# Kernel tuning notes

Measured on AMD Instinct MI355X. Metric: run time of the kernel, lower is better.

The kernel has to match this reference:

```python
import jax, jax.numpy as jnp
import numpy as np
import math

B, N, DIM = 4, 1024, 512
H, DH = 8, 64
INNER = H * DH
K_REG, TEMP = 0.3, 0.1
LARGE_NEG = -math.log(1e10)


def setup_inputs() -> dict:
    key = jax.random.key(0)
    ks = jax.random.split(key, 10)
    x = jax.random.normal(ks[0], (B, N, DIM), dtype=jnp.float32)
    # binary float mask [b, n, n]; keep diagonal on so every row has a positive pair
    mask = (jax.random.uniform(ks[1], (B, N, N)) < 0.5).astype(jnp.float32)
    mask = jnp.maximum(mask, jnp.eye(N, dtype=jnp.float32)[None])
    s_in = 1.0 / math.sqrt(DIM)
    s_out = 1.0 / math.sqrt(INNER)
    u = lambda k, shape, s: jax.random.uniform(k, shape, jnp.float32, -s, s)
    return {
        "x": x, "attn_mask": mask,
        "Wq": u(ks[2], (INNER, DIM), s_in), "bq": u(ks[3], (INNER,), s_in),
        "Wk": u(ks[4], (INNER, DIM), s_in), "bk": u(ks[5], (INNER,), s_in),
        "Wv": u(ks[6], (INNER, DIM), s_in), "bv": u(ks[7], (INNER,), s_in),
        "Wo": u(ks[8], (DIM, INNER), s_out), "bo": u(ks[9], (DIM,), s_out),
    }


def _dynamical_contrastive_loss(scores, attn_mask, norm_matrix):
    # reconstructed from CARD's DynamicalContrastiveLoss(k, temperature)
    n = scores.shape[-1]
    cos = scores / norm_matrix / TEMP                     # [b,h,n,n]
    m = jnp.max(cos, axis=-1, keepdims=True)              # stable exp; ratio unchanged
    e = jnp.exp(cos - m)
    amask = attn_mask[:, None]                            # [b,1,n,n]
    pos = jnp.sum(e * amask, axis=-1)                     # [b,h,n]
    allsum = jnp.sum(e, axis=-1)
    clustering = -jnp.log(pos / allsum)                   # [b,h,n]
    eye = jnp.eye(n, dtype=scores.dtype)
    regular = jnp.sum(jnp.abs(eye[None] - attn_mask), axis=(-2, -1)) / (n * (n - 1))  # [b]
    loss = jnp.mean(clustering, axis=(1, 2)) + K_REG * regular
    return jnp.mean(loss)


def reference(x, attn_mask, Wq, bq, Wk, bk, Wv, bv, Wo, bo):
    b, n, _ = x.shape
    split = lambda t: t.reshape(b, n, H, DH).transpose(0, 2, 1, 3)  # b h n d
    q = split(x @ Wq.T + bq)
    k = split(x @ Wk.T + bk)
    v = split(x @ Wv.T + bv)
    scores = jnp.einsum("bhid,bhjd->bhij", q, k)
    q_norm = jnp.linalg.norm(q, axis=-1, keepdims=True)   # [b,h,n,1]
    k_norm = jnp.linalg.norm(k, axis=-1, keepdims=True)
    norm_matrix = q_norm * jnp.swapaxes(k_norm, -1, -2)   # [b,h,n,n]
    amask = attn_mask[:, None]                            # [b,1,n,n]
    masked_scores = scores * amask + jnp.where(amask == 0, LARGE_NEG, 0.0)
    dcl = _dynamical_contrastive_loss(scores, attn_mask, norm_matrix)
    scale = 1.0 / math.sqrt(DH)
    attn = jax.nn.softmax(masked_scores * scale, axis=-1)
    out = jnp.einsum("bhij,bhjd->bhid", attn, v)
    out = out.transpose(0, 2, 1, 3).reshape(b, n, INNER)
    out = out @ Wo.T + bo                                 # dropout is identity at eval
    return out, attn, dcl
```

## Files before the change

### kernel.cpp

```cpp
#include <hip/hip_runtime.h>
#include <hip/hip_bf16.h>
#include <math.h>

#define NB 4
#define NN 1024
#define DIMD 512
#define NH 8
#define DHD 64
#define INNERD 512
#define SCALE 0.125f
#define TEMPP 0.1f
#define KREG 0.3f
#define LNEG -23.025850929940457f

typedef __attribute__((ext_vector_type(8))) short bf16x8;
typedef __attribute__((ext_vector_type(4))) short bf16x4;
typedef __attribute__((ext_vector_type(4))) float f32x4;

static __device__ __forceinline__ short f2bf(float f) {
  unsigned u = __float_as_uint(f);
  u += 0x7fffu + ((u >> 16) & 1u);
  return (short)(u >> 16);
}
static __device__ __forceinline__ float bf2f(short s) {
  unsigned u = ((unsigned)(unsigned short)s) << 16;
  return __uint_as_float(u);
}

static __device__ __forceinline__ float wave_sum(float v) {
#pragma unroll
  for (int o = 1; o < 64; o <<= 1) v += __shfl_xor(v, o, 64);
  return v;
}
static __device__ __forceinline__ float wave_min(float v) {
#pragma unroll
  for (int o = 1; o < 64; o <<= 1) v = fminf(v, __shfl_xor(v, o, 64));
  return v;
}

__global__ __launch_bounds__(256) void k_qkv(
    const float* __restrict__ x,
    const float* __restrict__ Wq, const float* __restrict__ bq,
    const float* __restrict__ Wk, const float* __restrict__ bk,
    const float* __restrict__ Wv, const float* __restrict__ bv,
    short* __restrict__ Qb, short* __restrict__ Kb, short* __restrict__ Vb,
    float* __restrict__ qn, float* __restrict__ kn) {
  __shared__ __align__(16) short As[64][40];
  __shared__ __align__(16) short Bs[64][40];
  const int tid = threadIdx.x;
  const int lane = tid & 63;
  const int wv = tid >> 6;
  const int m0 = blockIdx.x * 64;
  const int oc = blockIdx.y;
  const int which = oc >> 3;
  const int h = oc & 7;
  const float* W = (which == 0) ? Wq : (which == 1) ? Wk : Wv;
  const float* bias = (which == 0) ? bq : (which == 1) ? bk : bv;
  short* Out = (which == 0) ? Qb : (which == 1) ? Kb : Vb;
  const int o0 = h * 64;

  const f32x4 zero4 = {0.f, 0.f, 0.f, 0.f};
  f32x4 acc[4] = {zero4, zero4, zero4, zero4};

  const int sr = tid >> 3;
  const int sc = (tid & 7) * 4;

  for (int ks = 0; ks < 16; ++ks) {
    const int k0 = ks * 32;
    __syncthreads();
#pragma unroll
    for (int t = 0; t < 2; ++t) {
      const int r = sr + t * 32;
      const f32x4 va = *reinterpret_cast<const f32x4*>(&x[(m0 + r) * DIMD + k0 + sc]);
      const f32x4 vb = *reinterpret_cast<const f32x4*>(&W[(o0 + r) * DIMD + k0 + sc]);
      bf16x4 pa, pb;
#pragma unroll
      for (int i2 = 0; i2 < 4; ++i2) { pa[i2] = f2bf(va[i2]); pb[i2] = f2bf(vb[i2]); }
      *reinterpret_cast<bf16x4*>(&As[r][sc]) = pa;
      *reinterpret_cast<bf16x4*>(&Bs[r][sc]) = pb;
    }
    __syncthreads();
    const int kk = (lane >> 4) * 8;
    const bf16x8 a = *reinterpret_cast<const bf16x8*>(&As[wv * 16 + (lane & 15)][kk]);
#pragma unroll
    for (int n = 0; n < 4; ++n) {
      const bf16x8 b = *reinterpret_cast<const bf16x8*>(&Bs[n * 16 + (lane & 15)][kk]);
      acc[n] = __builtin_amdgcn_mfma_f32_16x16x32_bf16(a, b, acc[n], 0, 0, 0);
    }
  }

  const int colb = lane & 15;
  const int rbase = m0 + wv * 16 + ((lane >> 4) << 2);
  const int bidx = m0 >> 10;
  const int hb = (bidx * NH + h) << 10;
  float p2[4] = {0.f, 0.f, 0.f, 0.f};
#pragma unroll
  for (int n = 0; n < 4; ++n) {
    const float bval = bias[o0 + n * 16 + colb];
#pragma unroll
    for (int i = 0; i < 4; ++i) {
      const float val = acc[n][i] + bval;
      p2[i] += val * val;
      const int m = rbase + i;
      Out[(long)(hb + (m & (NN - 1))) * DHD + n * 16 + colb] = f2bf(val);
    }
  }
  if (which < 2) {
    float* norm = (which == 0) ? qn : kn;
#pragma unroll
    for (int off = 1; off < 16; off <<= 1) {
#pragma unroll
      for (int i = 0; i < 4; ++i) p2[i] += __shfl_xor(p2[i], off, 64);
    }
    if (colb == 0) {
#pragma unroll
      for (int i = 0; i < 4; ++i) {
        const int m = rbase + i;
        const float nv = sqrtf(p2[i]);
        norm[hb + (m & (NN - 1))] = (which == 0) ? (1.0f / (nv * TEMPP)) : (1.0f / nv);
      }
    }
  }
}

__global__ __launch_bounds__(256) void k_vtrans(const short* __restrict__ Vb,
                                                short* __restrict__ VbT) {
  __shared__ __align__(16) short T[64][72];
  const int tid = threadIdx.x;
  const int bh = blockIdx.y;
  const int j0 = blockIdx.x * 64;
#pragma unroll
  for (int t = 0; t < 2; ++t) {
    const int idx = tid + 256 * t;
    const int r = idx >> 3, c8 = (idx & 7) * 8;
    *reinterpret_cast<bf16x8*>(&T[r][c8]) =
        *reinterpret_cast<const bf16x8*>(&Vb[(long)((bh << 10) + j0 + r) * DHD + c8]);
  }
  __syncthreads();
  const int d = tid & 63;
  const int cg = tid >> 6;
#pragma unroll
  for (int t = 0; t < 2; ++t) {
    const int ch = cg * 2 + t;
    bf16x8 v;
#pragma unroll
    for (int jj = 0; jj < 8; ++jj) v[jj] = T[ch * 8 + jj][d];
    *reinterpret_cast<bf16x8*>(&VbT[((long)(bh * DHD + d) << 10) + j0 + ch * 8]) = v;
  }
}

__global__ __launch_bounds__(256) void k_kmax(const float* __restrict__ kn,
                                              float* __restrict__ kms) {
  const int tid = threadIdx.x;
  const int bh = blockIdx.x;
  const f32x4 v = *reinterpret_cast<const f32x4*>(&kn[(bh << 10) + tid * 4]);
  float m = fminf(fminf(v[0], v[1]), fminf(v[2], v[3]));
  m = wave_min(m);
  __shared__ float red[4];
  if ((tid & 63) == 0) red[tid >> 6] = m;
  __syncthreads();
  if (tid == 0) {
    const float mn = fminf(fminf(red[0], red[1]), fminf(red[2], red[3]));
    kms[bh] = (1.0f / mn) * SCALE / TEMPP;
  }
}

static __device__ __forceinline__ short* sp(short* S, int r, int c) {
  return (short*)((char*)S + (((r << 11) + (c << 1)) ^ ((r & 7) << 4)));
}

__global__ __launch_bounds__(256) void k_attn(
    const short* __restrict__ Qb, const short* __restrict__ Kb,
    const short* __restrict__ VbT,
    const float* __restrict__ mask,
    const float* __restrict__ qn, const float* __restrict__ kn,
    const float* __restrict__ kms,
    float* __restrict__ attn, short* __restrict__ AVb,
    float* __restrict__ partial, float* __restrict__ partial2) {
  __shared__ short S[16 * 1024];
  __shared__ float red[4][16][3];
  __shared__ float redc[4][16];
  __shared__ float rowv[16];
  __shared__ float rowscale[16];
  __shared__ float rowc[16];
  const int tid = threadIdx.x;
  const int lane = tid & 63;
  const int wv = tid >> 6;
  const int i0 = blockIdx.x * 16;
  const int bh = blockIdx.y;
  const int b = bh >> 3, h = bh & 7;

  const int lr = lane & 15;
  const int lk = lane >> 4;

  const long qoff = (long)((bh << 10) + i0 + lr) * DHD + lk * 8;
  const bf16x8 q0 = *reinterpret_cast<const bf16x8*>(&Qb[qoff]);
  const bf16x8 q1 = *reinterpret_cast<const bf16x8*>(&Qb[qoff + 32]);
  const short* Kbase = &Kb[(long)(bh << 10) * DHD];
  const float* mrow = mask + ((long)b << 20) + ((long)(i0 + lr) << 10);
  const float* knr = kn + (bh << 10);
  const float inv_qt = qn[(bh << 10) + i0 + lr];
  const float mlb = kms[bh] / inv_qt;
  const float argM = LNEG * SCALE - mlb;

  float Z = 0.f, alls = 0.f, pos = 0.f, cntf = 0.f;
#pragma unroll
  for (int jt = 0; jt < 16; ++jt) {
    const int j0 = wv * 256 + jt * 16;
    const long koff = (long)(j0 + lr) * DHD + lk * 8;
    const bf16x8 k0 = *reinterpret_cast<const bf16x8*>(&Kbase[koff]);
    const bf16x8 k1 = *reinterpret_cast<const bf16x8*>(&Kbase[koff + 32]);
    f32x4 acc = {0.f, 0.f, 0.f, 0.f};
    acc = __builtin_amdgcn_mfma_f32_16x16x32_bf16(k0, q0, acc, 0, 0, 0);
    acc = __builtin_amdgcn_mfma_f32_16x16x32_bf16(k1, q1, acc, 0, 0, 0);
    const int jl = j0 + lk * 4;
    const f32x4 mv = *reinterpret_cast<const f32x4*>(&mrow[jl]);
    const f32x4 kv = *reinterpret_cast<const f32x4*>(&knr[jl]);
    bf16x4 p;
#pragma unroll
    for (int e = 0; e < 4; ++e) {
      const float s = acc[e];
      const bool mset = (mv[e] != 0.0f);
      const float ev = __expf(mset ? (s * SCALE - mlb) : argM);
      const float ec = __expf(__builtin_fmaf(s * inv_qt, kv[e], -1.0f / TEMPP));
      Z += ev;
      alls += ec;
      pos += mset ? ec : 0.0f;
      cntf += mset ? 1.0f : 0.0f;
      p[e] = f2bf(ev);
    }
    *reinterpret_cast<bf16x4*>(sp(S, lr, jl)) = p;
  }
  Z += __shfl_xor(Z, 16, 64);    Z += __shfl_xor(Z, 32, 64);
  alls += __shfl_xor(alls, 16, 64); alls += __shfl_xor(alls, 32, 64);
  pos += __shfl_xor(pos, 16, 64);  pos += __shfl_xor(pos, 32, 64);
  if (lk == 0) { red[wv][lr][0] = Z; red[wv][lr][1] = alls; red[wv][lr][2] = pos; }
  if (h == 0) {
    cntf += __shfl_xor(cntf, 16, 64); cntf += __shfl_xor(cntf, 32, 64);
    if (lk == 0) redc[wv][lr] = cntf;
  }
  __syncthreads();

  const int r = tid >> 4, sub = tid & 15;
  if (sub == 0) {
    const float Zt = red[0][r][0] + red[1][r][0] + red[2][r][0] + red[3][r][0];
    const float at = red[0][r][1] + red[1][r][1] + red[2][r][1] + red[3][r][1];
    const float pt = red[0][r][2] + red[1][r][2] + red[2][r][2] + red[3][r][2];
    rowscale[r] = 1.0f / Zt;
    rowv[r] = __logf(at) - __logf(pt);
    if (h == 0) rowc[r] = redc[0][r] + redc[1][r] + redc[2][r] + redc[3][r];
  }
  __syncthreads();

  const float rZ = rowscale[r];
  float* arow = attn + ((long)bh << 20) + ((long)(i0 + r) << 10);
#pragma unroll
  for (int k = 0; k < 8; ++k) {
    const int c0 = sub * 8 + k * 128;
    const bf16x8 sv = *reinterpret_cast<const bf16x8*>(sp(S, r, c0));
    f32x4 o0, o1;
#pragma unroll
    for (int e = 0; e < 4; ++e) {
      o0[e] = bf2f(sv[e]) * rZ;
      o1[e] = bf2f(sv[4 + e]) * rZ;
    }
    *reinterpret_cast<f32x4*>(&arow[c0]) = o0;
    *reinterpret_cast<f32x4*>(&arow[c0 + 4]) = o1;
  }
  if (tid == 0) {
    float s = 0.f;
#pragma unroll
    for (int i = 0; i < 16; ++i) s += rowv[i];
    partial[bh * 64 + blockIdx.x] = s;
    if (h == 0) {
      float c = 0.f;
#pragma unroll
      for (int i = 0; i < 16; ++i) c += rowc[i];
      partial2[b * 64 + blockIdx.x] = c - 16.0f;
    }
  }

  f32x4 acc2 = {0.f, 0.f, 0.f, 0.f};
  const short* vrow = &VbT[(long)(bh * DHD + wv * 16 + lr) << 10];
#pragma unroll 8
  for (int k0 = 0; k0 < 32; ++k0) {
    const bf16x8 a = *reinterpret_cast<const bf16x8*>(sp(S, lr, k0 * 32 + lk * 8));
    const bf16x8 bb = *reinterpret_cast<const bf16x8*>(&vrow[k0 * 32 + lk * 8]);
    acc2 = __builtin_amdgcn_mfma_f32_16x16x32_bf16(a, bb, acc2, 0, 0, 0);
  }
#pragma unroll
  for (int i = 0; i < 4; ++i) {
    const int row = lk * 4 + i;
    const float o = acc2[i] * rowscale[row];
    AVb[((long)((b << 10) + i0 + row) << 9) + h * DHD + wv * 16 + lr] = f2bf(o);
  }
}

__global__ __launch_bounds__(256) void k_outproj(const short* __restrict__ AVb,
                                                 const float* __restrict__ Wo,
                                                 const float* __restrict__ bo,
                                                 float* __restrict__ out) {
  __shared__ __align__(16) short As[64][40];
  __shared__ __align__(16) short Bs[64][40];
  const int tid = threadIdx.x;
  const int lane = tid & 63, wv = tid >> 6;
  const int m0 = blockIdx.x * 64, o0 = blockIdx.y * 64;
  const f32x4 zero4 = {0.f, 0.f, 0.f, 0.f};
  f32x4 acc[4] = {zero4, zero4, zero4, zero4};
  const int ar = tid >> 2, ac = (tid & 3) * 8;
  const int br2 = tid >> 3, bc4 = (tid & 7) * 4;

  for (int ks = 0; ks < 16; ++ks) {
    const int k0 = ks * 32;
    __syncthreads();
    *reinterpret_cast<bf16x8*>(&As[ar][ac]) =
        *reinterpret_cast<const bf16x8*>(&AVb[((long)(m0 + ar) << 9) + k0 + ac]);
#pragma unroll
    for (int t = 0; t < 2; ++t) {
      const int rr = br2 + t * 32;
      const f32x4 vb = *reinterpret_cast<const f32x4*>(&Wo[(o0 + rr) * DIMD + k0 + bc4]);
      bf16x4 pbv;
#pragma unroll
      for (int i2 = 0; i2 < 4; ++i2) pbv[i2] = f2bf(vb[i2]);
      *reinterpret_cast<bf16x4*>(&Bs[rr][bc4]) = pbv;
    }
    __syncthreads();
    const int kk = (lane >> 4) * 8;
    const bf16x8 a = *reinterpret_cast<const bf16x8*>(&As[wv * 16 + (lane & 15)][kk]);
#pragma unroll
    for (int n = 0; n < 4; ++n) {
      const bf16x8 b = *reinterpret_cast<const bf16x8*>(&Bs[n * 16 + (lane & 15)][kk]);
      acc[n] = __builtin_amdgcn_mfma_f32_16x16x32_bf16(a, b, acc[n], 0, 0, 0);
    }
  }
  const int rbase = m0 + wv * 16 + ((lane >> 4) << 2);
#pragma unroll
  for (int i = 0; i < 4; ++i) {
#pragma unroll
    for (int n = 0; n < 4; ++n) {
      const int o = o0 + n * 16 + (lane & 15);
      out[((long)(rbase + i) << 9) + o] = acc[n][i] + bo[o];
    }
  }
}

__global__ __launch_bounds__(256) void k_finalize(const float* __restrict__ partial,
                                                  const float* __restrict__ partial2,
                                                  float* __restrict__ dcl) {
  const int tid = threadIdx.x;
  float s = 0.f;
#pragma unroll
  for (int t = 0; t < 8; ++t) s += partial[tid + t * 256];
  float s2 = partial2[tid];
  s = wave_sum(s);
  s2 = wave_sum(s2);
  __shared__ float red[4], red2[4];
  if ((tid & 63) == 0) { red[tid >> 6] = s; red2[tid >> 6] = s2; }
  __syncthreads();
  if (tid == 0) {
    const float cl = red[0] + red[1] + red[2] + red[3];
    const float rg = red2[0] + red2[1] + red2[2] + red2[3];
    *dcl = cl / (float)(NB * NH * NN) + KREG * rg / ((float)NN * (float)(NN - 1)) / (float)NB;
  }
}

extern "C" void kernel_launch(void* const* d_in, const int* in_sizes, int n_in,
                              void* d_out, int out_size, void* d_ws, size_t ws_size,
                              hipStream_t stream) {
  const float* x = (const float*)d_in[0];
  const float* mask = (const float*)d_in[1];
  const float* Wq = (const float*)d_in[2];
  const float* bq = (const float*)d_in[3];
  const float* Wk = (const float*)d_in[4];
  const float* bk = (const float*)d_in[5];
  const float* Wv = (const float*)d_in[6];
  const float* bv = (const float*)d_in[7];
  const float* Wo = (const float*)d_in[8];
  const float* bo = (const float*)d_in[9];

  float* out = (float*)d_out;
  float* attn = out + (size_t)NB * NN * DIMD;
  float* dcl = attn + (size_t)NB * NH * NN * NN;

  char* ws = (char*)d_ws;
  short* Qb = (short*)(ws);
  short* Kb = (short*)(ws + ((size_t)4 << 20));
  short* Vb = (short*)(ws + ((size_t)8 << 20));
  short* VbT = (short*)(ws + ((size_t)12 << 20));
  short* AVb = (short*)(ws + ((size_t)16 << 20));
  float* qn = (float*)(ws + ((size_t)20 << 20));
  float* kn = (float*)(ws + ((size_t)20 << 20) + (1 << 18));
  float* kms = (float*)(ws + ((size_t)20 << 20) + (2 << 18));
  float* partial = (float*)(ws + ((size_t)20 << 20) + (3 << 18));
  float* partial2 = (float*)(ws + ((size_t)20 << 20) + (4 << 18));

  k_qkv<<<dim3(64, 24), 256, 0, stream>>>(x, Wq, bq, Wk, bk, Wv, bv, Qb, Kb, Vb, qn, kn);
  k_vtrans<<<dim3(16, 32), 256, 0, stream>>>(Vb, VbT);
  k_kmax<<<dim3(32), 256, 0, stream>>>(kn, kms);
  k_attn<<<dim3(64, 32), 256, 0, stream>>>(Qb, Kb, VbT, mask, qn, kn, kms, attn, AVb,
                                           partial, partial2);
  k_outproj<<<dim3(64, 8), 256, 0, stream>>>(AVb, Wo, bo, out);
  k_finalize<<<1, 256, 0, stream>>>(partial, partial2, dcl);
}
```

Baseline: 303.2 us.

## Pre-convert inputs to bf16 and fuse V transpose and key-norm min into QKV GEMM

Adds a pre-pass that converts x and all weight matrices to bf16 once. The QKV GEMM becomes a larger 128x128-tile kernel that reads bf16 operands straight from global memory without LDS staging. That kernel also writes V directly in transposed layout and computes the per-head minimum key inverse norm with atomicMin, which removes the separate transpose and kmax kernels. The output projection likewise reads pre-converted bf16 Wo without shared memory. The cost is an extra conversion kernel plus a memset, and strided transposed V stores from the GEMM epilogue.

```diff
diff --git a/kernel.cpp b/kernel.cpp
--- a/kernel.cpp
+++ b/kernel.cpp
@@ -32,136 +32,130 @@
   for (int o = 1; o < 64; o <<= 1) v += __shfl_xor(v, o, 64);
   return v;
 }
-static __device__ __forceinline__ float wave_min(float v) {
-#pragma unroll
-  for (int o = 1; o < 64; o <<= 1) v = fminf(v, __shfl_xor(v, o, 64));
-  return v;
-}
-
-__global__ __launch_bounds__(256) void k_qkv(
-    const float* __restrict__ x,
-    const float* __restrict__ Wq, const float* __restrict__ bq,
-    const float* __restrict__ Wk, const float* __restrict__ bk,
-    const float* __restrict__ Wv, const float* __restrict__ bv,
-    short* __restrict__ Qb, short* __restrict__ Kb, short* __restrict__ Vb,
-    float* __restrict__ qn, float* __restrict__ kn) {
-  __shared__ __align__(16) short As[64][40];
-  __shared__ __align__(16) short Bs[64][40];
+
+__global__ __launch_bounds__(256) void k_pre(
+    const float* __restrict__ x, const float* __restrict__ Wq,
+    const float* __restrict__ Wk, const float* __restrict__ Wv,
+    const float* __restrict__ Wo,
+    short* __restrict__ xb, short* __restrict__ WB, short* __restrict__ WoB) {
+  const int idx = blockIdx.x * 256 + threadIdx.x;
+  const float* src;
+  short* dst;
+  int soff, doff;
+  if (idx < 524288) {
+    src = x; dst = xb; soff = doff = idx * 4;
+  } else if (idx < 720896) {
+    const int j = idx - 524288;
+    const int ww = j >> 16;
+    src = (ww == 0) ? Wq : (ww == 1) ? Wk : Wv;
+    soff = (j & 65535) * 4;
+    dst = WB; doff = j * 4;
+  } else {
+    const int j = idx - 720896;
+    src = Wo; dst = WoB; soff = doff = j * 4;
+  }
+  const f32x4 v = *reinterpret_cast<const f32x4*>(&src[soff]);
+  bf16x4 p;
+#pragma unroll
+  for (int e = 0; e < 4; ++e) p[e] = f2bf(v[e]);
+  *reinterpret_cast<bf16x4*>(&dst[doff]) = p;
+}
+
+__global__ __launch_bounds__(256) void k_qkv2(
+    const short* __restrict__ xb, const short* __restrict__ WB,
+    const float* __restrict__ bq, const float* __restrict__ bk,
+    const float* __restrict__ bv,
+    short* __restrict__ Qb, short* __restrict__ Kb, short* __restrict__ VbT,
+    float* __restrict__ qn, float* __restrict__ kn,
+    unsigned* __restrict__ kminU) {
   const int tid = threadIdx.x;
   const int lane = tid & 63;
-  const int wv = tid >> 6;
-  const int m0 = blockIdx.x * 64;
-  const int oc = blockIdx.y;
-  const int which = oc >> 3;
-  const int h = oc & 7;
-  const float* W = (which == 0) ? Wq : (which == 1) ? Wk : Wv;
+  const int w = tid >> 6;
+  const int wr = w >> 1, wc = w & 1;
+  const int lr = lane & 15, lk = lane >> 4;
+  const int m0 = blockIdx.x * 128;
+  const int n0 = blockIdx.y * 128;
+
+  const short* abase = &xb[(long)(m0 + wr * 64 + lr) * DIMD + lk * 8];
+  const short* bbase = &WB[(long)(n0 + wc * 64 + lr) * DIMD + lk * 8];
+
+  const f32x4 z4 = {0.f, 0.f, 0.f, 0.f};
+  f32x4 acc[4][4] = {{z4, z4, z4, z4}, {z4, z4, z4, z4},
+                     {z4, z4, z4, z4}, {z4, z4, z4, z4}};
+
+  for (int ks = 0; ks < 16; ++ks) {
+    const int ko = ks * 32;
+    bf16x8 af[4], bfr[4];
+#pragma unroll
+    for (int t = 0; t < 4; ++t) {
+      af[t] = *reinterpret_cast<const bf16x8*>(&abase[t * 16 * DIMD + ko]);
+      bfr[t] = *reinterpret_cast<const bf16x8*>(&bbase[t * 16 * DIMD + ko]);
+    }
+#pragma unroll
+    for (int ar = 0; ar < 4; ++ar)
+#pragma unroll
+      for (int ac = 0; ac < 4; ++ac)
+        acc[ar][ac] =
+            __builtin_amdgcn_mfma_f32_16x16x32_bf16(af[ar], bfr[ac], acc[ar][ac], 0, 0, 0);
+  }
+
+  const int ncb = n0 + wc * 64;
+  const int which = ncb >> 9;
+  const int h = (ncb >> 6) & 7;
+  const int b = m0 >> 10;
+  const int bh = b * NH + h;
   const float* bias = (which == 0) ? bq : (which == 1) ? bk : bv;
-  short* Out = (which == 0) ? Qb : (which == 1) ? Kb : Vb;
-  const int o0 = h * 64;
-
-  const f32x4 zero4 = {0.f, 0.f, 0.f, 0.f};
-  f32x4 acc[4] = {zero4, zero4, zero4, zero4};
-
-  const int sr = tid >> 3;
-  const int sc = (tid & 7) * 4;
-
-  for (int ks = 0; ks < 16; ++ks) {
-    const int k0 = ks * 32;
-    __syncthreads();
-#pragma unroll
-    for (int t = 0; t < 2; ++t) {
-      const int r = sr + t * 32;
-      const f32x4 va = *reinterpret_cast<const f32x4*>(&x[(m0 + r) * DIMD + k0 + sc]);
-      const f32x4 vb = *reinterpret_cast<const f32x4*>(&W[(o0 + r) * DIMD + k0 + sc]);
-      bf16x4 pa, pb;
-#pragma unroll
-      for (int i2 = 0; i2 < 4; ++i2) { pa[i2] = f2bf(va[i2]); pb[i2] = f2bf(vb[i2]); }
-      *reinterpret_cast<bf16x4*>(&As[r][sc]) = pa;
-      *reinterpret_cast<bf16x4*>(&Bs[r][sc]) = pb;
-    }
-    __syncthreads();
-    const int kk = (lane >> 4) * 8;
-    const bf16x8 a = *reinterpret_cast<const bf16x8*>(&As[wv * 16 + (lane & 15)][kk]);
-#pragma unroll
-    for (int n = 0; n < 4; ++n) {
-      const bf16x8 b = *reinterpret_cast<const bf16x8*>(&Bs[n * 16 + (lane & 15)][kk]);
-      acc[n] = __builtin_amdgcn_mfma_f32_16x16x32_bf16(a, b, acc[n], 0, 0, 0);
-    }
-  }
-
-  const int colb = lane & 15;
-  const int rbase = m0 + wv * 16 + ((lane >> 4) << 2);
-  const int bidx = m0 >> 10;
-  const int hb = (bidx * NH + h) << 10;
-  float p2[4] = {0.f, 0.f, 0.f, 0.f};
-#pragma unroll
-  for (int n = 0; n < 4; ++n) {
-    const float bval = bias[o0 + n * 16 + colb];
-#pragma unroll
-    for (int i = 0; i < 4; ++i) {
-      const float val = acc[n][i] + bval;
-      p2[i] += val * val;
-      const int m = rbase + i;
-      Out[(long)(hb + (m & (NN - 1))) * DHD + n * 16 + colb] = f2bf(val);
-    }
-  }
+  short* Out = (which == 0) ? Qb : Kb;
+  const int rbase = (m0 & (NN - 1)) + wr * 64 + lk * 4;
+
+  float p2[4][4];
+#pragma unroll
+  for (int ar = 0; ar < 4; ++ar)
+#pragma unroll
+    for (int i = 0; i < 4; ++i) p2[ar][i] = 0.f;
+
+#pragma unroll
+  for (int ac = 0; ac < 4; ++ac) {
+    const int d = ac * 16 + lr;
+    const float bval = bias[h * 64 + d];
+#pragma unroll
+    for (int ar = 0; ar < 4; ++ar) {
+#pragma unroll
+      for (int i = 0; i < 4; ++i) {
+        const float val = acc[ar][ac][i] + bval;
+        p2[ar][i] += val * val;
+        const int rowIn = rbase + ar * 16 + i;
+        if (which < 2) {
+          Out[((long)((bh << 10) + rowIn) << 6) + d] = f2bf(val);
+        } else {
+          VbT[((long)((bh << 6) + d) << 10) + rowIn] = f2bf(val);
+        }
+      }
+    }
+  }
+
   if (which < 2) {
     float* norm = (which == 0) ? qn : kn;
 #pragma unroll
-    for (int off = 1; off < 16; off <<= 1) {
-#pragma unroll
-      for (int i = 0; i < 4; ++i) p2[i] += __shfl_xor(p2[i], off, 64);
-    }
-    if (colb == 0) {
-#pragma unroll
-      for (int i = 0; i < 4; ++i) {
-        const int m = rbase + i;
-        const float nv = sqrtf(p2[i]);
-        norm[hb + (m & (NN - 1))] = (which == 0) ? (1.0f / (nv * TEMPP)) : (1.0f / nv);
+    for (int off = 1; off < 16; off <<= 1)
+#pragma unroll
+      for (int ar = 0; ar < 4; ++ar)
+#pragma unroll
+        for (int i = 0; i < 4; ++i) p2[ar][i] += __shfl_xor(p2[ar][i], off, 64);
+    if (lr == 0) {
+      float lmin = 3.4e38f;
+#pragma unroll
+      for (int ar = 0; ar < 4; ++ar) {
+#pragma unroll
+        for (int i = 0; i < 4; ++i) {
+          const int rowIn = rbase + ar * 16 + i;
+          const float inv = 1.0f / sqrtf(p2[ar][i]);
+          norm[(bh << 10) + rowIn] = (which == 0) ? (inv / TEMPP) : inv;
+          lmin = fminf(lmin, inv);
+        }
       }
-    }
-  }
-}
-
-__global__ __launch_bounds__(256) void k_vtrans(const short* __restrict__ Vb,
-                                                short* __restrict__ VbT) {
-  __shared__ __align__(16) short T[64][72];
-  const int tid = threadIdx.x;
-  const int bh = blockIdx.y;
-  const int j0 = blockIdx.x * 64;
-#pragma unroll
-  for (int t = 0; t < 2; ++t) {
-    const int idx = tid + 256 * t;
-    const int r = idx >> 3, c8 = (idx & 7) * 8;
-    *reinterpret_cast<bf16x8*>(&T[r][c8]) =
-        *reinterpret_cast<const bf16x8*>(&Vb[(long)((bh << 10) + j0 + r) * DHD + c8]);
-  }
-  __syncthreads();
-  const int d = tid & 63;
-  const int cg = tid >> 6;
-#pragma unroll
-  for (int t = 0; t < 2; ++t) {
-    const int ch = cg * 2 + t;
-    bf16x8 v;
-#pragma unroll
-    for (int jj = 0; jj < 8; ++jj) v[jj] = T[ch * 8 + jj][d];
-    *reinterpret_cast<bf16x8*>(&VbT[((long)(bh * DHD + d) << 10) + j0 + ch * 8]) = v;
-  }
-}
-
-__global__ __launch_bounds__(256) void k_kmax(const float* __restrict__ kn,
-                                              float* __restrict__ kms) {
-  const int tid = threadIdx.x;
-  const int bh = blockIdx.x;
-  const f32x4 v = *reinterpret_cast<const f32x4*>(&kn[(bh << 10) + tid * 4]);
-  float m = fminf(fminf(v[0], v[1]), fminf(v[2], v[3]));
-  m = wave_min(m);
-  __shared__ float red[4];
-  if ((tid & 63) == 0) red[tid >> 6] = m;
-  __syncthreads();
-  if (tid == 0) {
-    const float mn = fminf(fminf(red[0], red[1]), fminf(red[2], red[3]));
-    kms[bh] = (1.0f / mn) * SCALE / TEMPP;
+      if (which == 1) atomicMin(&kminU[bh], __float_as_uint(lmin));
+    }
   }
 }
 
@@ -174,7 +168,7 @@
     const short* __restrict__ VbT,
     const float* __restrict__ mask,
     const float* __restrict__ qn, const float* __restrict__ kn,
-    const float* __restrict__ kms,
+    const unsigned* __restrict__ kminU,
     float* __restrict__ attn, short* __restrict__ AVb,
     float* __restrict__ partial, float* __restrict__ partial2) {
   __shared__ short S[16 * 1024];
@@ -200,7 +194,8 @@
   const float* mrow = mask + ((long)b << 20) + ((long)(i0 + lr) << 10);
   const float* knr = kn + (bh << 10);
   const float inv_qt = qn[(bh << 10) + i0 + lr];
-  const float mlb = kms[bh] / inv_qt;
+  const float kminv = __uint_as_float(kminU[bh]);
+  const float mlb = (SCALE / TEMPP) / (kminv * inv_qt);
   const float argM = LNEG * SCALE - mlb;
 
   float Z = 0.f, alls = 0.f, pos = 0.f, cntf = 0.f;
@@ -296,50 +291,38 @@
   }
 }
 
-__global__ __launch_bounds__(256) void k_outproj(const short* __restrict__ AVb,
-                                                 const float* __restrict__ Wo,
-                                                 const float* __restrict__ bo,
-                                                 float* __restrict__ out) {
-  __shared__ __align__(16) short As[64][40];
-  __shared__ __align__(16) short Bs[64][40];
+__global__ __launch_bounds__(256) void k_outproj2(const short* __restrict__ AVb,
+                                                  const short* __restrict__ WoB,
+                                                  const float* __restrict__ bo,
+                                                  float* __restrict__ out) {
   const int tid = threadIdx.x;
-  const int lane = tid & 63, wv = tid >> 6;
-  const int m0 = blockIdx.x * 64, o0 = blockIdx.y * 64;
-  const f32x4 zero4 = {0.f, 0.f, 0.f, 0.f};
-  f32x4 acc[4] = {zero4, zero4, zero4, zero4};
-  const int ar = tid >> 2, ac = (tid & 3) * 8;
-  const int br2 = tid >> 3, bc4 = (tid & 7) * 4;
+  const int lane = tid & 63;
+  const int w = tid >> 6;
+  const int lr = lane & 15, lk = lane >> 4;
+  const int m0 = blockIdx.x * 64 + w * 16;
+  const int n0 = blockIdx.y * 64;
+  const short* abase = &AVb[(long)(m0 + lr) * INNERD + lk * 8];
+  const short* bbase = &WoB[(long)(n0 + lr) * INNERD + lk * 8];
+  const f32x4 z4 = {0.f, 0.f, 0.f, 0.f};
+  f32x4 acc[4] = {z4, z4, z4, z4};
 
   for (int ks = 0; ks < 16; ++ks) {
-    const int k0 = ks * 32;
-    __syncthreads();
-    *reinterpret_cast<bf16x8*>(&As[ar][ac]) =
-        *reinterpret_cast<const bf16x8*>(&AVb[((long)(m0 + ar) << 9) + k0 + ac]);
-#pragma unroll
-    for (int t = 0; t < 2; ++t) {
-      const int rr = br2 + t * 32;
-      const f32x4 vb = *reinterpret_cast<const f32x4*>(&Wo[(o0 + rr) * DIMD + k0 + bc4]);
-      bf16x4 pbv;
-#pragma unroll
-      for (int i2 = 0; i2 < 4; ++i2) pbv[i2] = f2bf(vb[i2]);
-      *reinterpret_cast<bf16x4*>(&Bs[rr][bc4]) = pbv;
-    }
-    __syncthreads();
-    const int kk = (lane >> 4) * 8;
-    const bf16x8 a = *reinterpret_cast<const bf16x8*>(&As[wv * 16 + (lane & 15)][kk]);
-#pragma unroll
-    for (int n = 0; n < 4; ++n) {
-      const bf16x8 b = *reinterpret_cast<const bf16x8*>(&Bs[n * 16 + (lane & 15)][kk]);
-      acc[n] = __builtin_amdgcn_mfma_f32_16x16x32_bf16(a, b, acc[n], 0, 0, 0);
-    }
-  }
-  const int rbase = m0 + wv * 16 + ((lane >> 4) << 2);
-#pragma unroll
-  for (int i = 0; i < 4; ++i) {
-#pragma unroll
-    for (int n = 0; n < 4; ++n) {
-      const int o = o0 + n * 16 + (lane & 15);
-      out[((long)(rbase + i) << 9) + o] = acc[n][i] + bo[o];
+    const int ko = ks * 32;
+    const bf16x8 af = *reinterpret_cast<const bf16x8*>(&abase[ko]);
+#pragma unroll
+    for (int ac = 0; ac < 4; ++ac) {
+      const bf16x8 bf = *reinterpret_cast<const bf16x8*>(&bbase[ac * 16 * INNERD + ko]);
+      acc[ac] = __builtin_amdgcn_mfma_f32_16x16x32_bf16(af, bf, acc[ac], 0, 0, 0);
+    }
+  }
+#pragma unroll
+  for (int ac = 0; ac < 4; ++ac) {
+    const int n = n0 + ac * 16 + lr;
+    const float bv = bo[n];
+#pragma unroll
+    for (int i = 0; i < 4; ++i) {
+      const int m = m0 + lk * 4 + i;
+      out[((long)m << 9) + n] = acc[ac][i] + bv;
     }
   }
 }
@@ -385,20 +368,24 @@
   char* ws = (char*)d_ws;
   short* Qb = (short*)(ws);
   short* Kb = (short*)(ws + ((size_t)4 << 20));
-  short* Vb = (short*)(ws + ((size_t)8 << 20));
-  short* VbT = (short*)(ws + ((size_t)12 << 20));
-  short* AVb = (short*)(ws + ((size_t)16 << 20));
-  float* qn = (float*)(ws + ((size_t)20 << 20));
-  float* kn = (float*)(ws + ((size_t)20 << 20) + (1 << 18));
-  float* kms = (float*)(ws + ((size_t)20 << 20) + (2 << 18));
-  float* partial = (float*)(ws + ((size_t)20 << 20) + (3 << 18));
-  float* partial2 = (float*)(ws + ((size_t)20 << 20) + (4 << 18));
-
-  k_qkv<<<dim3(64, 24), 256, 0, stream>>>(x, Wq, bq, Wk, bk, Wv, bv, Qb, Kb, Vb, qn, kn);
-  k_vtrans<<<dim3(16, 32), 256, 0, stream>>>(Vb, VbT);
-  k_kmax<<<dim3(32), 256, 0, stream>>>(kn, kms);
-  k_attn<<<dim3(64, 32), 256, 0, stream>>>(Qb, Kb, VbT, mask, qn, kn, kms, attn, AVb,
+  short* VbT = (short*)(ws + ((size_t)8 << 20));
+  short* xb = (short*)(ws + ((size_t)12 << 20));
+  short* AVb = xb;
+  short* WB = (short*)(ws + ((size_t)16 << 20));
+  short* WoB = (short*)(ws + ((size_t)16 << 20) + 1572864);
+  char* tail = ws + ((size_t)18 << 20);
+  float* qn = (float*)(tail);
+  float* kn = (float*)(tail + (128 << 10));
+  unsigned* kminU = (unsigned*)(tail + (256 << 10));
+  float* partial = (float*)(tail + (320 << 10));
+  float* partial2 = (float*)(tail + (384 << 10));
+
+  hipMemsetAsync(kminU, 0xFF, 32 * sizeof(unsigned), stream);
+
+  k_pre<<<dim3(3072), 256, 0, stream>>>(x, Wq, Wk, Wv, Wo, xb, WB, WoB);
+  k_qkv2<<<dim3(32, 12), 256, 0, stream>>>(xb, WB, bq, bk, bv, Qb, Kb, VbT, qn, kn, kminU);
+  k_attn<<<dim3(64, 32), 256, 0, stream>>>(Qb, Kb, VbT, mask, qn, kn, kminU, attn, AVb,
                                            partial, partial2);
-  k_outproj<<<dim3(64, 8), 256, 0, stream>>>(AVb, Wo, bo, out);
+  k_outproj2<<<dim3(64, 8), 256, 0, stream>>>(AVb, WoB, bo, out);
   k_finalize<<<1, 256, 0, stream>>>(partial, partial2, dcl);
 }
```

Result: slower. 316.0 us (+4.2%).
